# Kernel optimization log

Measured on AMD Instinct MI355X. Metric: run time of the kernel, lower is better.

The kernel has to match this reference:

```python
import jax, jax.numpy as jnp
import numpy as np

LEAK = 0.1
EPS = 1e-5

N, C, T, V = 32, 64, 400, 27
S, IC, O = 2, 16, 64  # num_subset, inter_channels, out_channels


def _make_pe(channel, joint_num, time_len):
    pos = np.tile(np.arange(joint_num), time_len).astype(np.float32)[:, None]
    div = np.exp(np.arange(0, channel, 2).astype(np.float32) * (-(np.log(10000.0) / channel)))
    pe = np.zeros((time_len * joint_num, channel), np.float32)
    pe[:, 0::2] = np.sin(pos * div)
    pe[:, 1::2] = np.cos(pos * div)
    # (T*V, C) -> (1, C, T, V)
    return jnp.asarray(pe.reshape(time_len, joint_num, channel).transpose(2, 0, 1)[None])


def setup_inputs() -> dict:
    key = jax.random.key(0)
    ks = jax.random.split(key, 16)
    w = lambda k, shp, fan: jax.random.normal(k, shp, jnp.float32) * (1.0 / np.sqrt(fan))
    inp = {
        "x": jax.random.normal(ks[0], (N, C, T, V), jnp.float32),
        "pe": _make_pe(C, V, T),
        # in_nets: Conv2d(C, 2*S*IC, 1)
        "W_in": w(ks[1], (2 * S * IC, C), C),
        "b_in": jnp.zeros((2 * S * IC,), jnp.float32),
        "alphas": jnp.ones((1, S, 1, 1), jnp.float32),
        "att0": jnp.ones((1, S, V, V), jnp.float32) / V,
        # out_nets: Conv2d(S*C, O, 1) + BN
        "W_out": w(ks[2], (O, S * C), S * C),
        "b_out": jnp.zeros((O,), jnp.float32),
        "g_out": jnp.ones((O,), jnp.float32),
        "be_out": jnp.zeros((O,), jnp.float32),
        "m_out": jax.random.normal(ks[3], (O,), jnp.float32) * 0.1,
        "v_out": jax.random.uniform(ks[4], (O,), jnp.float32, 0.5, 1.5),
        # ff_nets: Conv2d(O, O, 1) + BN
        "W_ff": w(ks[5], (O, O), O),
        "b_ff": jnp.zeros((O,), jnp.float32),
        "g_ff": jnp.ones((O,), jnp.float32),
        "be_ff": jnp.zeros((O,), jnp.float32),
        "m_ff": jax.random.normal(ks[6], (O,), jnp.float32) * 0.1,
        "v_ff": jax.random.uniform(ks[7], (O,), jnp.float32, 0.5, 1.5),
        # out_nett: Conv2d(O, O, (3,1), pad (1,0)) + BN
        "W_t": w(ks[8], (O, O, 3, 1), O * 3),
        "b_t": jnp.zeros((O,), jnp.float32),
        "g_t": jnp.ones((O,), jnp.float32),
        "be_t": jnp.zeros((O,), jnp.float32),
        "m_t": jax.random.normal(ks[9], (O,), jnp.float32) * 0.1,
        "v_t": jax.random.uniform(ks[10], (O,), jnp.float32, 0.5, 1.5),
    }
    return inp


def _lrelu(x):
    return jnp.where(x >= 0, x, LEAK * x)


def _bn(x, g, b, m, v):
    scale = g / jnp.sqrt(v + EPS)
    return (x - m[None, :, None, None]) * scale[None, :, None, None] + b[None, :, None, None]


def _conv1x1(x, W, b):
    return jnp.einsum('oc,nctv->notv', W, x) + b[None, :, None, None]


def reference(x, pe, W_in, b_in, alphas, att0, W_out, b_out, g_out, be_out, m_out, v_out,
              W_ff, b_ff, g_ff, be_ff, m_ff, v_ff, W_t, b_t, g_t, be_t, m_t, v_t):
    n, c, t, v_ = x.shape
    s = alphas.shape[1]
    ic = W_in.shape[0] // (2 * s)
    # positional encoding on the attention-input branch only
    y = x + pe[:, :, :t]
    qk = _conv1x1(y, W_in, b_in).reshape(n, 2 * s, ic, t, v_)
    q, k = qk[:, :s], qk[:, s:]
    # atts buffer is zeros; dropout is identity in eval
    att = jnp.tanh(jnp.einsum('nsctu,nsctv->nsuv', q, k) / (ic * t)) * alphas + att0
    y = jnp.einsum('nctu,nsuv->nsctv', x, att).reshape(n, s * c, t, v_)
    y = _bn(_conv1x1(y, W_out, b_out), g_out, be_out, m_out, v_out)
    y = _lrelu(x + y)  # downs1 = identity
    yf = _bn(_conv1x1(y, W_ff, b_ff), g_ff, be_ff, m_ff, v_ff)
    y = _lrelu(x + yf)  # downs2 = identity
    z = jax.lax.conv_general_dilated(
        y, W_t, window_strides=(1, 1), padding=((1, 1), (0, 0)),
        dimension_numbers=('NCHW', 'OIHW', 'NCHW'))
    z = _bn(z + b_t[None, :, None, None], g_t, be_t, m_t, v_t)
    z = _lrelu(y + z)  # downt2 = identity
    return z
```

## Files before the change

kernel.cpp:

```cpp
#include <hip/hip_runtime.h>
#include <hip/hip_bf16.h>

typedef __hip_bfloat16 bf16;
typedef unsigned short u16;
typedef __attribute__((ext_vector_type(8))) short short8;
typedef __attribute__((ext_vector_type(4))) short s4v;
typedef __attribute__((ext_vector_type(4))) float f32x4;
typedef __attribute__((ext_vector_type(4))) unsigned int u32x4;

#define LEAK 0.1f
#define EPS_ 1e-5f
#define MFMA(a, b, c) __builtin_amdgcn_mfma_f32_16x16x32_bf16(a, b, c, 0, 0, 0)

__device__ __forceinline__ float u2f(u16 u) { return __uint_as_float(((unsigned int)u) << 16); }
__device__ __forceinline__ u16 f2u(float f) {
  bf16 h = __float2bfloat16(f);
  u16 r;
  __builtin_memcpy(&r, &h, 2);
  return r;
}
__device__ __forceinline__ f32x4 z4() { f32x4 z = {0.f, 0.f, 0.f, 0.f}; return z; }

__global__ __launch_bounds__(512, 2) void g_qk(
    const float* __restrict__ x, const float* __restrict__ pe,
    const float* __restrict__ W_in, const float* __restrict__ b_in,
    u16* __restrict__ qG, u16* __restrict__ kG)
{
  __shared__ __align__(16) u16 sB16[16 * 2 * 64 * 8];
  const int tid = threadIdx.x;
  const int w = tid >> 6, lane = tid & 63;
  const int m = lane & 15, quad = lane >> 4;
  const int ot = w & 3, g = w >> 2;
  const int n = blockIdx.y, p0 = blockIdx.x * 256;

  short8 aW[2];
#pragma unroll
  for (int kf = 0; kf < 2; ++kf) {
    short8 tt;
#pragma unroll
    for (int j = 0; j < 8; ++j)
      tt[j] = (short)f2u(W_in[(16 * ot + m) * 64 + 32 * kf + 8 * quad + j]);
    aW[kf] = tt;
  }
  float bb[4];
#pragma unroll
  for (int r = 0; r < 4; ++r) bb[r] = b_in[16 * ot + quad * 4 + r];

#pragma unroll
  for (int i = 0; i < 4; ++i) {
    int unit = i * 512 + tid;
    int c = unit >> 5, poct = unit & 31;
    int p = p0 + poct * 8;
    const float* xp = &x[(n * 64 + c) * 10800 + p];
    const float* pp = &pe[c * 10800 + p];
    float xv[8];
    if (p + 7 < 10800) {
      *(f32x4*)&xv[0] = *(const f32x4*)xp;
      *(f32x4*)&xv[4] = *(const f32x4*)(xp + 4);
      f32x4 pv0 = *(const f32x4*)pp;
      f32x4 pv1 = *(const f32x4*)(pp + 4);
#pragma unroll
      for (int e = 0; e < 4; ++e) { xv[e] += pv0[e]; xv[4 + e] += pv1[e]; }
    } else {
#pragma unroll
      for (int e = 0; e < 8; ++e)
        xv[e] = (p + e < 10800) ? xp[e] + pp[e] : 0.f;
    }
    int kf = c >> 5, qq = (c >> 3) & 3, j = c & 7;
#pragma unroll
    for (int e = 0; e < 8; ++e) {
      int pl = poct * 8 + e;
      int tile = pl >> 4, mm = pl & 15;
      sB16[(((tile * 2 + kf) * 64) + qq * 16 + mm) * 8 + j] = f2u(xv[e]);
    }
  }
  __syncthreads();

  u16* dst = (ot < 2 ? qG : kG) + (n * 2 + (ot & 1)) * 32 * 6400;
#pragma unroll 4
  for (int ti = 0; ti < 8; ++ti) {
    int tile = 8 * g + ti;
    short8 b0 = *(const short8*)&sB16[((tile * 2 + 0) * 64 + lane) * 8];
    short8 b1 = *(const short8*)&sB16[((tile * 2 + 1) * 64 + lane) * 8];
    f32x4 acc = MFMA(aW[0], b0, z4());
    acc = MFMA(aW[1], b1, acc);
    int p = p0 + tile * 16 + m;
    if (p < 10800) {
      unsigned t = (unsigned)p / 27u;
      unsigned u = (unsigned)p - 27u * t;
      s4v pk;
#pragma unroll
      for (int reg = 0; reg < 4; ++reg) pk[reg] = (short)f2u(acc[reg] + bb[reg]);
      *(s4v*)&dst[(u * 400 + t) * 16 + quad * 4] = pk;
    }
  }
}

__global__ __launch_bounds__(256) void g_att_part(
    const u16* __restrict__ qG, const u16* __restrict__ kG,
    float* __restrict__ att)
{
  __shared__ float sred[4][64][16];
  const int tid = threadIdx.x;
  const int w = tid >> 6, lane = tid & 63;
  const int m = lane & 15, quad = lane >> 4;
  const int s = blockIdx.x / 25, kc = blockIdx.x % 25;
  const int n = blockIdx.y;
  const u16* qb = qG + (n * 2 + s) * 32 * 6400;
  const u16* kb = kG + (n * 2 + s) * 32 * 6400;

  f32x4 a00 = z4(), a01 = z4(), a10 = z4(), a11 = z4();
  const int kk0 = kc * 256 + w * 64;
#pragma unroll
  for (int kf = 0; kf < 2; ++kf) {
    int kk = kk0 + kf * 32 + quad * 8;
    short8 aq0 = *(const short8*)&qb[m * 6400 + kk];
    short8 aq1 = *(const short8*)&qb[(16 + m) * 6400 + kk];
    short8 bk0 = *(const short8*)&kb[m * 6400 + kk];
    short8 bk1 = *(const short8*)&kb[(16 + m) * 6400 + kk];
    a00 = MFMA(aq0, bk0, a00);
    a01 = MFMA(aq0, bk1, a01);
    a10 = MFMA(aq1, bk0, a10);
    a11 = MFMA(aq1, bk1, a11);
  }
  *(f32x4*)&sred[w][lane][0] = a00;
  *(f32x4*)&sred[w][lane][4] = a01;
  *(f32x4*)&sred[w][lane][8] = a10;
  *(f32x4*)&sred[w][lane][12] = a11;
  __syncthreads();
#pragma unroll
  for (int k = 0; k < 4; ++k) {
    int slot = tid + 256 * k;
    int lsrc = slot >> 4, idx = slot & 15;
    float val = sred[0][lsrc][idx] + sred[1][lsrc][idx] +
                sred[2][lsrc][idx] + sred[3][lsrc][idx];
    int f = idx >> 2, reg = idx & 3;
    int ut = f >> 1, vt = f & 1;
    int qq = lsrc >> 4, mm = lsrc & 15;
    int u = ut * 16 + qq * 4 + reg, v = vt * 16 + mm;
    if (u < 27 && v < 27)
      atomicAdd(&att[(n * 2 + s) * 729 + u * 27 + v], val);
  }
}

__global__ __launch_bounds__(256) void k_att_fin(
    float* __restrict__ att, const float* __restrict__ alphas,
    const float* __restrict__ att0)
{
  int i = blockIdx.x * 256 + threadIdx.x;
  if (i >= 32 * 2 * 729) return;
  int s = (i / 729) & 1;
  int r = i % 729;
  att[i] = tanhf(att[i] * (1.f / 6400.f)) * alphas[s] + att0[s * 729 + r];
}

__global__ __launch_bounds__(512, 2) void g_ab(
    const float* __restrict__ x, const float* __restrict__ att,
    const float* __restrict__ W_out, const float* __restrict__ b_out,
    const float* __restrict__ g_out, const float* __restrict__ be_out,
    const float* __restrict__ m_out, const float* __restrict__ v_out,
    u16* __restrict__ y3T)
{
  __shared__ u32x4 sy2f[4][2][4][64];
  const int tid = threadIdx.x;
  const int w = tid >> 6, lane = tid & 63;
  const int m = lane & 15, quad = lane >> 4;
  const int ot = w & 3, g = w >> 2;
  const int n = blockIdx.y, t0 = blockIdx.x * 4;

  float axr[2][8];
#pragma unroll
  for (int li = 0; li < 2; ++li) {
    int t = t0 + 2 * li + g;
    const float* xp = &x[((n * 64 + 16 * ot + m) * 400 + t) * 27];
#pragma unroll
    for (int j = 0; j < 8; ++j) {
      int u = quad * 8 + j;
      axr[li][j] = (u < 27) ? xp[u] : 0.f;
    }
  }
  float xres[2][2][4];
#pragma unroll
  for (int ci = 0; ci < 2; ++ci) {
    int t = t0 + 2 * ci + g;
#pragma unroll
    for (int vt = 0; vt < 2; ++vt) {
      int v = vt * 16 + m;
#pragma unroll
      for (int reg = 0; reg < 4; ++reg) {
        int o = 16 * ot + quad * 4 + reg;
        xres[ci][vt][reg] = (v < 27) ? x[((n * 64 + o) * 400 + t) * 27 + v] : 0.f;
      }
    }
  }

  short8 bAtt[4];
#pragma unroll
  for (int s = 0; s < 2; ++s)
#pragma unroll
    for (int nt = 0; nt < 2; ++nt) {
      short8 tt;
#pragma unroll
      for (int j = 0; j < 8; ++j) {
        int u = 8 * quad + j, v = 16 * nt + m;
        tt[j] = (u < 27 && v < 27) ? (short)f2u(att[(n * 2 + s) * 729 + u * 27 + v]) : (short)0;
      }
      bAtt[s * 2 + nt] = tt;
    }
  short8 aWo[4];
#pragma unroll
  for (int kf = 0; kf < 4; ++kf) {
    short8 tt;
#pragma unroll
    for (int j = 0; j < 8; ++j)
      tt[j] = (short)f2u(W_out[(16 * ot + m) * 128 + 32 * kf + 8 * quad + j]);
    aWo[kf] = tt;
  }
  float Ao[4], Bo[4];
#pragma unroll
  for (int reg = 0; reg < 4; ++reg) {
    int o = 16 * ot + quad * 4 + reg;
    float sc = g_out[o] * rsqrtf(v_out[o] + EPS_);
    Ao[reg] = sc;
    Bo[reg] = (b_out[o] - m_out[o]) * sc + be_out[o];
  }

  const int q1 = quad & 1;
  const int qp = (2 * ot + (quad >> 1)) & 3;
#pragma unroll
  for (int li = 0; li < 2; ++li) {
    int tc = 2 * li + g;
    short8 ax;
#pragma unroll
    for (int j = 0; j < 8; ++j) ax[j] = (short)f2u(axr[li][j]);
    f32x4 acc[4];
#pragma unroll
    for (int f = 0; f < 4; ++f) acc[f] = MFMA(ax, bAtt[f], z4());
#pragma unroll
    for (int s = 0; s < 2; ++s)
#pragma unroll
      for (int nt = 0; nt < 2; ++nt) {
        f32x4 a = acc[s * 2 + nt];
        s4v pk;
#pragma unroll
        for (int reg = 0; reg < 4; ++reg) pk[reg] = (short)f2u(a[reg]);
        int kfp = 2 * s + (ot >> 1);
        *(s4v*)((u16*)&sy2f[tc][nt][kfp][qp * 16 + m] + 4 * q1) = pk;
      }
  }
  __syncthreads();
#pragma unroll
  for (int ci = 0; ci < 2; ++ci) {
    int tc = 2 * ci + g;
    int t = t0 + tc;
#pragma unroll
    for (int vt = 0; vt < 2; ++vt) {
      f32x4 a0 = z4();
#pragma unroll
      for (int kf = 0; kf < 4; ++kf) {
        short8 b = *(const short8*)&sy2f[tc][vt][kf][lane];
        a0 = MFMA(aWo[kf], b, a0);
      }
      int v = vt * 16 + m;
      if (v < 27) {
        s4v pk;
#pragma unroll
        for (int reg = 0; reg < 4; ++reg) {
          float r = xres[ci][vt][reg] + a0[reg] * Ao[reg] + Bo[reg];
          pk[reg] = (short)f2u((r >= 0.f) ? r : LEAK * r);
        }
        *(s4v*)&y3T[(unsigned)(n * 10800 + t * 27 + v) * 64 + 16 * ot + quad * 4] = pk;
      }
    }
  }
}

__global__ __launch_bounds__(512, 2) void g_cd(
    const float* __restrict__ x, const u16* __restrict__ y3T,
    const float* __restrict__ W_ff, const float* __restrict__ b_ff,
    const float* __restrict__ g_ff, const float* __restrict__ be_ff,
    const float* __restrict__ m_ff, const float* __restrict__ v_ff,
    const float* __restrict__ W_t, const float* __restrict__ b_t,
    const float* __restrict__ g_t, const float* __restrict__ be_t,
    const float* __restrict__ m_t, const float* __restrict__ v_t,
    float* __restrict__ out)
{
  __shared__ u32x4 sy4f[10][2][2][64];
  const int tid = threadIdx.x;
  const int w = tid >> 6, lane = tid & 63;
  const int m = lane & 15, quad = lane >> 4;
  const int ot = w & 3, g = w >> 2;
  const int n = blockIdx.y, t0 = blockIdx.x * 8;

  short8 aWf[2], aWt[6];
#pragma unroll
  for (int kf = 0; kf < 2; ++kf) {
    short8 tt;
#pragma unroll
    for (int j = 0; j < 8; ++j)
      tt[j] = (short)f2u(W_ff[(16 * ot + m) * 64 + 32 * kf + 8 * quad + j]);
    aWf[kf] = tt;
  }
#pragma unroll
  for (int kf = 0; kf < 6; ++kf) {
    short8 tt;
    int dt = kf >> 1;
#pragma unroll
    for (int j = 0; j < 8; ++j) {
      int ii = 32 * (kf & 1) + 8 * quad + j;
      tt[j] = (short)f2u(W_t[((16 * ot + m) * 64 + ii) * 3 + dt]);
    }
    aWt[kf] = tt;
  }
  float Af[4], Bf[4], At[4], Bt[4];
#pragma unroll
  for (int reg = 0; reg < 4; ++reg) {
    int o = 16 * ot + quad * 4 + reg;
    float sc;
    sc = g_ff[o] * rsqrtf(v_ff[o] + EPS_); Af[reg] = sc; Bf[reg] = (b_ff[o] - m_ff[o]) * sc + be_ff[o];
    sc = g_t[o] * rsqrtf(v_t[o] + EPS_);   At[reg] = sc; Bt[reg] = (b_t[o] - m_t[o]) * sc + be_t[o];
  }

  const int q1 = quad & 1;
  const int qp = (2 * ot + (quad >> 1)) & 3;
  const int kfp = ot >> 1;
#pragma unroll
  for (int li = 0; li < 5; ++li) {
    int tl = 2 * li + g;
    int t = t0 - 1 + tl;
    if (t >= 0 && t < 400) {
      short8 yb[2][2];
      float xr[2][4];
#pragma unroll
      for (int vt = 0; vt < 2; ++vt) {
        int v = vt * 16 + m;
        unsigned p = (unsigned)(n * 10800 + t * 27 + v);
        yb[vt][0] = *(const short8*)&y3T[p * 64 + quad * 8];
        yb[vt][1] = *(const short8*)&y3T[p * 64 + 32 + quad * 8];
#pragma unroll
        for (int reg = 0; reg < 4; ++reg) {
          int o = 16 * ot + quad * 4 + reg;
          xr[vt][reg] = (v < 27) ? x[((n * 64 + o) * 400 + t) * 27 + v] : 0.f;
        }
      }
#pragma unroll
      for (int vt = 0; vt < 2; ++vt) {
        f32x4 acc = MFMA(aWf[0], yb[vt][0], z4());
        acc = MFMA(aWf[1], yb[vt][1], acc);
        s4v pk;
#pragma unroll
        for (int reg = 0; reg < 4; ++reg) {
          float r = xr[vt][reg] + acc[reg] * Af[reg] + Bf[reg];
          pk[reg] = (short)f2u((r >= 0.f) ? r : LEAK * r);
        }
        *(s4v*)((u16*)&sy4f[tl][vt][kfp][qp * 16 + m] + 4 * q1) = pk;
      }
    } else {
      s4v zz = {0, 0, 0, 0};
#pragma unroll
      for (int vt = 0; vt < 2; ++vt)
        *(s4v*)((u16*)&sy4f[tl][vt][kfp][qp * 16 + m] + 4 * q1) = zz;
    }
  }
  __syncthreads();
#pragma unroll
  for (int ci = 0; ci < 4; ++ci) {
    int tc = 2 * ci + g;
    int t = t0 + tc;
#pragma unroll
    for (int vt = 0; vt < 2; ++vt) {
      f32x4 acc = z4();
#pragma unroll
      for (int kf = 0; kf < 6; ++kf) {
        short8 b = *(const short8*)&sy4f[tc + (kf >> 1)][vt][kf & 1][lane];
        acc = MFMA(aWt[kf], b, acc);
      }
      int v = vt * 16 + m;
      if (v < 27) {
        s4v res = *(const s4v*)((const u16*)&sy4f[tc + 1][vt][kfp][qp * 16 + m] + 4 * q1);
#pragma unroll
        for (int reg = 0; reg < 4; ++reg) {
          int o = 16 * ot + quad * 4 + reg;
          float r = u2f((u16)res[reg]) + acc[reg] * At[reg] + Bt[reg];
          out[((n * 64 + o) * 400 + t) * 27 + v] = (r >= 0.f) ? r : LEAK * r;
        }
      }
    }
  }
}

extern "C" void kernel_launch(void* const* d_in, const int* in_sizes, int n_in,
                              void* d_out, int out_size, void* d_ws, size_t ws_size,
                              hipStream_t stream)
{
  const float* x      = (const float*)d_in[0];
  const float* pe     = (const float*)d_in[1];
  const float* W_in   = (const float*)d_in[2];
  const float* b_in   = (const float*)d_in[3];
  const float* alphas = (const float*)d_in[4];
  const float* att0   = (const float*)d_in[5];
  const float* W_out  = (const float*)d_in[6];
  const float* b_out  = (const float*)d_in[7];
  const float* g_out  = (const float*)d_in[8];
  const float* be_out = (const float*)d_in[9];
  const float* m_out  = (const float*)d_in[10];
  const float* v_out  = (const float*)d_in[11];
  const float* W_ff   = (const float*)d_in[12];
  const float* b_ff   = (const float*)d_in[13];
  const float* g_ff   = (const float*)d_in[14];
  const float* be_ff  = (const float*)d_in[15];
  const float* m_ff   = (const float*)d_in[16];
  const float* v_ff   = (const float*)d_in[17];
  const float* W_t    = (const float*)d_in[18];
  const float* b_t    = (const float*)d_in[19];
  const float* g_t    = (const float*)d_in[20];
  const float* be_t   = (const float*)d_in[21];
  const float* m_t    = (const float*)d_in[22];
  const float* v_t    = (const float*)d_in[23];

  float* att = (float*)d_ws;
  u16* qG  = (u16*)((char*)d_ws + (1u << 20));
  u16* kG  = (u16*)((char*)d_ws + (1u << 20) + 26214400u);
  u16* y3T = (u16*)((char*)d_ws + (1u << 20));

  hipMemsetAsync(att, 0, 32 * 2 * 729 * sizeof(float), stream);
  g_qk<<<dim3(43, 32), 512, 0, stream>>>(x, pe, W_in, b_in, qG, kG);
  g_att_part<<<dim3(50, 32), 256, 0, stream>>>(qG, kG, att);
  k_att_fin<<<dim3(183), 256, 0, stream>>>(att, alphas, att0);
  g_ab<<<dim3(100, 32), 512, 0, stream>>>(
      x, att, W_out, b_out, g_out, be_out, m_out, v_out, y3T);
  g_cd<<<dim3(50, 32), 512, 0, stream>>>(
      x, y3T, W_ff, b_ff, g_ff, be_ff, m_ff, v_ff,
      W_t, b_t, g_t, be_t, m_t, v_t, (float*)d_out);
}
```

Baseline: 418.3 us.

## Fuse q/k projection with attention partial reduction, keep q/k in LDS

Merges the q/k 1x1 projection kernel and the attention partial-score kernel into one kernel. Each block now takes 216 positions (8 whole time steps of 27 joints), writes q/k into shared memory laid out by joint and time, and runs the q·kᵀ MFMA reduction in place before atomically adding into att. This removes the global round trip of the bf16 q/k buffers and one kernel launch. In exchange the input loads become scalar (no float4), the kernel uses more LDS, and there are more atomics per att entry (50 blocks per batch).

```diff
diff --git a/kernel.cpp b/kernel.cpp
--- a/kernel.cpp
+++ b/kernel.cpp
@@ -21,17 +21,20 @@
 }
 __device__ __forceinline__ f32x4 z4() { f32x4 z = {0.f, 0.f, 0.f, 0.f}; return z; }
 
-__global__ __launch_bounds__(512, 2) void g_qk(
+__global__ __launch_bounds__(512, 2) void g_qk_att(
     const float* __restrict__ x, const float* __restrict__ pe,
     const float* __restrict__ W_in, const float* __restrict__ b_in,
-    u16* __restrict__ qG, u16* __restrict__ kG)
-{
-  __shared__ __align__(16) u16 sB16[16 * 2 * 64 * 8];
+    float* __restrict__ att)
+{
+  __shared__ __align__(16) u16 sB16[14 * 2 * 64 * 8];
+  __shared__ __align__(16) u16 sQF[2][32][136];
+  __shared__ __align__(16) u16 sKF[2][32][136];
   const int tid = threadIdx.x;
   const int w = tid >> 6, lane = tid & 63;
   const int m = lane & 15, quad = lane >> 4;
   const int ot = w & 3, g = w >> 2;
-  const int n = blockIdx.y, p0 = blockIdx.x * 256;
+  const int n = blockIdx.y;
+  const int p0 = blockIdx.x * 216;
 
   short8 aW[2];
 #pragma unroll
@@ -46,100 +49,53 @@
 #pragma unroll
   for (int r = 0; r < 4; ++r) bb[r] = b_in[16 * ot + quad * 4 + r];
 
-#pragma unroll
-  for (int i = 0; i < 4; ++i) {
-    int unit = i * 512 + tid;
-    int c = unit >> 5, poct = unit & 31;
-    int p = p0 + poct * 8;
-    const float* xp = &x[(n * 64 + c) * 10800 + p];
-    const float* pp = &pe[c * 10800 + p];
-    float xv[8];
-    if (p + 7 < 10800) {
-      *(f32x4*)&xv[0] = *(const f32x4*)xp;
-      *(f32x4*)&xv[4] = *(const f32x4*)(xp + 4);
-      f32x4 pv0 = *(const f32x4*)pp;
-      f32x4 pv1 = *(const f32x4*)(pp + 4);
-#pragma unroll
-      for (int e = 0; e < 4; ++e) { xv[e] += pv0[e]; xv[4 + e] += pv1[e]; }
-    } else {
-#pragma unroll
-      for (int e = 0; e < 8; ++e)
-        xv[e] = (p + e < 10800) ? xp[e] + pp[e] : 0.f;
-    }
+#pragma unroll 4
+  for (int i = 0; i < 28; ++i) {
+    int idx = i * 512 + tid;
+    int c = idx / 224, pl = idx % 224;
+    float v = 0.f;
+    if (pl < 216)
+      v = x[(n * 64 + c) * 10800 + p0 + pl] + pe[c * 10800 + p0 + pl];
+    int tile = pl >> 4, mm = pl & 15;
     int kf = c >> 5, qq = (c >> 3) & 3, j = c & 7;
-#pragma unroll
-    for (int e = 0; e < 8; ++e) {
-      int pl = poct * 8 + e;
-      int tile = pl >> 4, mm = pl & 15;
-      sB16[(((tile * 2 + kf) * 64) + qq * 16 + mm) * 8 + j] = f2u(xv[e]);
-    }
+    sB16[(((tile * 2 + kf) * 64) + qq * 16 + mm) * 8 + j] = f2u(v);
   }
   __syncthreads();
 
-  u16* dst = (ot < 2 ? qG : kG) + (n * 2 + (ot & 1)) * 32 * 6400;
-#pragma unroll 4
-  for (int ti = 0; ti < 8; ++ti) {
-    int tile = 8 * g + ti;
+  u16* dstF = (ot < 2 ? &sQF[0][0][0] : &sKF[0][0][0]) + (ot & 1) * 32 * 136;
+#pragma unroll
+  for (int ti = 0; ti < 7; ++ti) {
+    int tile = 7 * g + ti;
     short8 b0 = *(const short8*)&sB16[((tile * 2 + 0) * 64 + lane) * 8];
     short8 b1 = *(const short8*)&sB16[((tile * 2 + 1) * 64 + lane) * 8];
     f32x4 acc = MFMA(aW[0], b0, z4());
     acc = MFMA(aW[1], b1, acc);
-    int p = p0 + tile * 16 + m;
-    if (p < 10800) {
-      unsigned t = (unsigned)p / 27u;
-      unsigned u = (unsigned)p - 27u * t;
+    int pl = tile * 16 + m;
+    if (pl < 216) {
+      int tl = pl / 27, u = pl - tl * 27;
       s4v pk;
 #pragma unroll
       for (int reg = 0; reg < 4; ++reg) pk[reg] = (short)f2u(acc[reg] + bb[reg]);
-      *(s4v*)&dst[(u * 400 + t) * 16 + quad * 4] = pk;
-    }
-  }
-}
-
-__global__ __launch_bounds__(256) void g_att_part(
-    const u16* __restrict__ qG, const u16* __restrict__ kG,
-    float* __restrict__ att)
-{
-  __shared__ float sred[4][64][16];
-  const int tid = threadIdx.x;
-  const int w = tid >> 6, lane = tid & 63;
-  const int m = lane & 15, quad = lane >> 4;
-  const int s = blockIdx.x / 25, kc = blockIdx.x % 25;
-  const int n = blockIdx.y;
-  const u16* qb = qG + (n * 2 + s) * 32 * 6400;
-  const u16* kb = kG + (n * 2 + s) * 32 * 6400;
-
-  f32x4 a00 = z4(), a01 = z4(), a10 = z4(), a11 = z4();
-  const int kk0 = kc * 256 + w * 64;
-#pragma unroll
-  for (int kf = 0; kf < 2; ++kf) {
-    int kk = kk0 + kf * 32 + quad * 8;
-    short8 aq0 = *(const short8*)&qb[m * 6400 + kk];
-    short8 aq1 = *(const short8*)&qb[(16 + m) * 6400 + kk];
-    short8 bk0 = *(const short8*)&kb[m * 6400 + kk];
-    short8 bk1 = *(const short8*)&kb[(16 + m) * 6400 + kk];
-    a00 = MFMA(aq0, bk0, a00);
-    a01 = MFMA(aq0, bk1, a01);
-    a10 = MFMA(aq1, bk0, a10);
-    a11 = MFMA(aq1, bk1, a11);
-  }
-  *(f32x4*)&sred[w][lane][0] = a00;
-  *(f32x4*)&sred[w][lane][4] = a01;
-  *(f32x4*)&sred[w][lane][8] = a10;
-  *(f32x4*)&sred[w][lane][12] = a11;
+      *(s4v*)&dstF[u * 136 + tl * 16 + quad * 4] = pk;
+    }
+  }
   __syncthreads();
-#pragma unroll
-  for (int k = 0; k < 4; ++k) {
-    int slot = tid + 256 * k;
-    int lsrc = slot >> 4, idx = slot & 15;
-    float val = sred[0][lsrc][idx] + sred[1][lsrc][idx] +
-                sred[2][lsrc][idx] + sred[3][lsrc][idx];
-    int f = idx >> 2, reg = idx & 3;
-    int ut = f >> 1, vt = f & 1;
-    int qq = lsrc >> 4, mm = lsrc & 15;
-    int u = ut * 16 + qq * 4 + reg, v = vt * 16 + mm;
-    if (u < 27 && v < 27)
-      atomicAdd(&att[(n * 2 + s) * 729 + u * 27 + v], val);
+
+  {
+    const int s = w & 1, ut = (w >> 1) & 1, vt = w >> 2;
+    f32x4 acc = z4();
+#pragma unroll
+    for (int ks = 0; ks < 4; ++ks) {
+      short8 a = *(const short8*)&sQF[s][ut * 16 + m][ks * 32 + quad * 8];
+      short8 b = *(const short8*)&sKF[s][vt * 16 + m][ks * 32 + quad * 8];
+      acc = MFMA(a, b, acc);
+    }
+#pragma unroll
+    for (int reg = 0; reg < 4; ++reg) {
+      int u = ut * 16 + quad * 4 + reg, v = vt * 16 + m;
+      if (u < 27 && v < 27)
+        atomicAdd(&att[(n * 2 + s) * 729 + u * 27 + v], acc[reg]);
+    }
   }
 }
 
@@ -419,13 +375,10 @@
   const float* v_t    = (const float*)d_in[23];
 
   float* att = (float*)d_ws;
-  u16* qG  = (u16*)((char*)d_ws + (1u << 20));
-  u16* kG  = (u16*)((char*)d_ws + (1u << 20) + 26214400u);
   u16* y3T = (u16*)((char*)d_ws + (1u << 20));
 
   hipMemsetAsync(att, 0, 32 * 2 * 729 * sizeof(float), stream);
-  g_qk<<<dim3(43, 32), 512, 0, stream>>>(x, pe, W_in, b_in, qG, kG);
-  g_att_part<<<dim3(50, 32), 256, 0, stream>>>(qG, kG, att);
+  g_qk_att<<<dim3(50, 32), 512, 0, stream>>>(x, pe, W_in, b_in, att);
   k_att_fin<<<dim3(183), 256, 0, stream>>>(att, alphas, att0);
   g_ab<<<dim3(100, 32), 512, 0, stream>>>(
       x, att, W_out, b_out, g_out, be_out, m_out, v_out, y3T);
```

Measured after the change: 430.8 us. +3.0%, slower.
